# Kernel optimization log

Measured on AMD Instinct MI355X. Metric: run time of the kernel, lower is better.

The kernel has to match this reference:

```python
import jax, jax.numpy as jnp
import numpy as np


def pnp(contour, h, w):
    """Even-odd point-in-polygon rasterization.
    contour: [P, N, 2] float (x, y) pixel coords -> [P, h, w] float {0,1} masks.
    Scans over the N polygon edges (fixed structural dim), toggling parity.
    """
    P, N, _ = contour.shape
    py = jnp.arange(h, dtype=contour.dtype)[:, None]   # [h, 1]
    px = jnp.arange(w, dtype=contour.dtype)[None, :]   # [1, w]
    verts = jnp.moveaxis(contour, 1, 0)                # [N, P, 2]
    nxt = jnp.roll(verts, -1, axis=0)                  # next vertex per edge

    def step(inside, vn):
        v, n = vn
        x1 = v[:, 0][:, None, None]; y1 = v[:, 1][:, None, None]
        x2 = n[:, 0][:, None, None]; y2 = n[:, 1][:, None, None]
        crosses = (y1 > py) != (y2 > py)               # edge straddles scanline
        denom = jnp.where(y2 == y1, 1.0, y2 - y1)
        xint = (x2 - x1) * (py - y1) / denom + x1      # x of edge at scanline
        hit = crosses & (px < xint)
        return inside ^ hit, None

    inside0 = jnp.zeros((P, h, w), dtype=bool)
    inside, _ = jax.lax.scan(step, inside0, (verts, nxt))
    return inside.astype(jnp.float32)


def setup_inputs() -> dict:
    key = jax.random.key(0)
    k1, k2, k3, k4 = jax.random.split(key, 4)
    bs, c_in, h, w = 8, 64, 256, 256
    P, num_point = 40, 128
    ct_num = jax.random.randint(k1, (bs,), 1, 16)  # at least one contour per image
    cx = jax.random.uniform(k2, (P, num_point), minval=0.0, maxval=float(w - 1))
    cy = jax.random.uniform(k3, (P, num_point), minval=0.0, maxval=float(h - 1))
    contour = jnp.stack([cx, cy], axis=-1)                     # [P, N, 2]
    cnn_feature = jax.random.normal(k4, (bs, c_in, h, w), dtype=jnp.float32)
    return {"contour": contour, "cnn_feature": cnn_feature, "ct_num": ct_num}


def reference(contour, cnn_feature, ct_num):
    bs, c_in, h, w = cnn_feature.shape
    mask = pnp(contour, h, w)                                  # [P, h, w]
    max_channel = int(jnp.max(ct_num))
    # Faithful to original: slice start for batch i>=1 is ct_num[i-1] (not cumsum)
    starts = jnp.concatenate([jnp.zeros((1,), ct_num.dtype), ct_num[:-1]])
    j = jnp.arange(max_channel)
    idx = starts[:, None] + j[None, :]                         # [bs, C]
    valid = j[None, :] < ct_num[:, None]                       # [bs, C]
    gathered = mask[jnp.clip(idx, 0, mask.shape[0] - 1)]       # [bs, C, h, w]
    mask_batch = jnp.where(valid[:, :, None, None], gathered, 0.0)
    max_mask = jnp.max(mask_batch, axis=1, keepdims=True)      # [bs, 1, h, w]
    cnn_out = jax.nn.relu(max_mask * cnn_feature + cnn_feature)
    return mask_batch, cnn_out
```

## Files before the change

### kernel.cpp

```cpp
#include <hip/hip_runtime.h>

#define P_NUM 40
#define N_VERT 128
#define H 256
#define W 256
#define BS 8
#define C_IN 64
#define PIX (H * W)
#define PIX4 (PIX / 4)
#define CSPLIT 4
#define CPS (C_IN / CSPLIT)

typedef float vf2 __attribute__((ext_vector_type(2)));
typedef float vf4 __attribute__((ext_vector_type(4)));

__global__ __launch_bounds__(256) void pnp_mask_kernel(
    const float* __restrict__ contour, float* __restrict__ maskws) {
    const int p = blockIdx.x;
    const int y = blockIdx.y;
    const int tid = threadIdx.x;

    __shared__ float sx[N_VERT];
    __shared__ float sy[N_VERT];
    __shared__ float xints[N_VERT];
    __shared__ int kcnt;

    if (tid < N_VERT) {
        const vf2 v = reinterpret_cast<const vf2*>(contour)[p * N_VERT + tid];
        sx[tid] = v.x;
        sy[tid] = v.y;
    }
    if (tid == 0) kcnt = 0;
    __syncthreads();

    const float py = (float)y;
    if (tid < N_VERT) {
        const float y1 = sy[tid];
        const int e2 = (tid + 1) & (N_VERT - 1);
        const float y2 = sy[e2];
        const bool crosses = (y1 > py) != (y2 > py);
        if (crosses) {
            const float x1 = sx[tid];
            const float x2 = sx[e2];
            const float denom = (y2 == y1) ? 1.0f : (y2 - y1);
            const float xint = (x2 - x1) * (py - y1) / denom + x1;
            const int slot = atomicAdd(&kcnt, 1);
            xints[slot] = xint;
        }
    }
    __syncthreads();

    const int K = kcnt;
    const float px = (float)tid;
    int cnt = 0;
    for (int k = 0; k < K; ++k) {
        cnt += (px < xints[k]) ? 1 : 0;
    }
    maskws[(p * H + y) * W + tid] = (float)(cnt & 1);
}

__global__ __launch_bounds__(256) void mega_kernel(
    const float* __restrict__ maskws, const float* __restrict__ feat,
    const int* __restrict__ ct_num, float* __restrict__ out_mask,
    float* __restrict__ out_cnn, int C) {
    const int bid = blockIdx.x;
    const int split = bid & (CSPLIT - 1);
    const int chunk = (bid >> 2) & 63;
    const int i = bid >> 8;
    const int qv = chunk * 256 + threadIdx.x;

    const int cn = ct_num[i];
    const int start = (i == 0) ? 0 : ct_num[i - 1];

    vf4 mx = {0.f, 0.f, 0.f, 0.f};
    if (split == 0) {
        for (int j = 0; j < C; ++j) {
            vf4 m = {0.f, 0.f, 0.f, 0.f};
            if (j < cn) {
                const int p = min(max(start + j, 0), P_NUM - 1);
                m = reinterpret_cast<const vf4*>(maskws)[p * PIX4 + qv];
                mx.x = fmaxf(mx.x, m.x);
                mx.y = fmaxf(mx.y, m.y);
                mx.z = fmaxf(mx.z, m.z);
                mx.w = fmaxf(mx.w, m.w);
            }
            __builtin_nontemporal_store(
                m, reinterpret_cast<vf4*>(out_mask) + (size_t)(i * C + j) * PIX4 + qv);
        }
    } else {
        for (int j = 0; j < cn; ++j) {
            const int p = min(max(start + j, 0), P_NUM - 1);
            const vf4 m = reinterpret_cast<const vf4*>(maskws)[p * PIX4 + qv];
            mx.x = fmaxf(mx.x, m.x);
            mx.y = fmaxf(mx.y, m.y);
            mx.z = fmaxf(mx.z, m.z);
            mx.w = fmaxf(mx.w, m.w);
        }
    }

    const int cbase = split * CPS;
    for (int cc = 0; cc < CPS; ++cc) {
        const size_t idx = (size_t)(i * C_IN + cbase + cc) * PIX4 + qv;
        const vf4 f = reinterpret_cast<const vf4*>(feat)[idx];
        vf4 r;
        r.x = fmaxf(mx.x * f.x + f.x, 0.0f);
        r.y = fmaxf(mx.y * f.y + f.y, 0.0f);
        r.z = fmaxf(mx.z * f.z + f.z, 0.0f);
        r.w = fmaxf(mx.w * f.w + f.w, 0.0f);
        __builtin_nontemporal_store(r, reinterpret_cast<vf4*>(out_cnn) + idx);
    }
}

extern "C" void kernel_launch(void* const* d_in, const int* in_sizes, int n_in,
                              void* d_out, int out_size, void* d_ws, size_t ws_size,
                              hipStream_t stream) {
    const float* contour = (const float*)d_in[0];
    const float* feat = (const float*)d_in[1];
    const int* ct_num = (const int*)d_in[2];

    float* out = (float*)d_out;
    const int cnn_elems = BS * C_IN * PIX;
    const int C = (out_size - cnn_elems) / (BS * PIX);

    float* maskws = (float*)d_ws;
    float* out_mask = out;
    float* out_cnn = out + (size_t)BS * C * PIX;

    hipLaunchKernelGGL(pnp_mask_kernel, dim3(P_NUM, H), dim3(256), 0, stream,
                       contour, maskws);

    hipLaunchKernelGGL(mega_kernel, dim3(BS * 64 * CSPLIT), dim3(256), 0, stream,
                       maskws, feat, ct_num, out_mask, out_cnn, C);
}
```

Before: 65.96 us.

## Pack polygon masks into bitmasks and split mask output into separate blocks

The rasterizer now writes one bit per pixel via wavefront ballot instead of a float per pixel, which shrinks the intermediate mask workspace 32x. The fused kernel ORs the packed words to form the max mask and expands the bits back to floats. The mask_batch output is moved out of split 0 into its own set of blocks, one per (batch, channel, chunk). The channel split is raised from 4 to 8. Together these cut workspace traffic and remove the serial store loop from a subset of blocks, at the cost of bit extraction work and a larger grid.

```diff
diff --git a/kernel.cpp b/kernel.cpp
--- a/kernel.cpp
+++ b/kernel.cpp
@@ -8,14 +8,15 @@
 #define C_IN 64
 #define PIX (H * W)
 #define PIX4 (PIX / 4)
-#define CSPLIT 4
-#define CPS (C_IN / CSPLIT)
+#define CHUNKS 64
+#define ASPLIT 8
+#define CPS (C_IN / ASPLIT)
 
 typedef float vf2 __attribute__((ext_vector_type(2)));
 typedef float vf4 __attribute__((ext_vector_type(4)));
 
-__global__ __launch_bounds__(256) void pnp_mask_kernel(
-    const float* __restrict__ contour, float* __restrict__ maskws) {
+__global__ __launch_bounds__(256) void pnp_bits_kernel(
+    const float* __restrict__ contour, unsigned int* __restrict__ bitws) {
     const int p = blockIdx.x;
     const int y = blockIdx.y;
     const int tid = threadIdx.x;
@@ -56,58 +57,83 @@
     for (int k = 0; k < K; ++k) {
         cnt += (px < xints[k]) ? 1 : 0;
     }
-    maskws[(p * H + y) * W + tid] = (float)(cnt & 1);
+    const unsigned long long b = __ballot(cnt & 1);
+    if ((tid & 63) == 0) {
+        *reinterpret_cast<unsigned long long*>(
+            bitws + ((size_t)(p * H + y) << 3) + ((tid >> 6) << 1)) = b;
+    }
 }
 
-__global__ __launch_bounds__(256) void mega_kernel(
-    const float* __restrict__ maskws, const float* __restrict__ feat,
+__device__ __forceinline__ vf4 expand_bits(unsigned int word, int sh) {
+    vf4 m;
+    m.x = ((word >> (sh + 0)) & 1u) ? 1.0f : 0.0f;
+    m.y = ((word >> (sh + 1)) & 1u) ? 1.0f : 0.0f;
+    m.z = ((word >> (sh + 2)) & 1u) ? 1.0f : 0.0f;
+    m.w = ((word >> (sh + 3)) & 1u) ? 1.0f : 0.0f;
+    return m;
+}
+
+__global__ __launch_bounds__(256) void fuse_expand_kernel(
+    const unsigned int* __restrict__ bitws, const float* __restrict__ feat,
     const int* __restrict__ ct_num, float* __restrict__ out_mask,
     float* __restrict__ out_cnn, int C) {
+    const int FUSE_BLOCKS = BS * CHUNKS * ASPLIT;
     const int bid = blockIdx.x;
-    const int split = bid & (CSPLIT - 1);
-    const int chunk = (bid >> 2) & 63;
-    const int i = bid >> 8;
-    const int qv = chunk * 256 + threadIdx.x;
+    const int tid = threadIdx.x;
 
-    const int cn = ct_num[i];
-    const int start = (i == 0) ? 0 : ct_num[i - 1];
+    if (bid < FUSE_BLOCKS) {
+        const int split = bid & (ASPLIT - 1);
+        const int chunk = (bid >> 3) & (CHUNKS - 1);
+        const int i = bid >> 9;
 
-    vf4 mx = {0.f, 0.f, 0.f, 0.f};
-    if (split == 0) {
-        for (int j = 0; j < C; ++j) {
-            vf4 m = {0.f, 0.f, 0.f, 0.f};
-            if (j < cn) {
-                const int p = min(max(start + j, 0), P_NUM - 1);
-                m = reinterpret_cast<const vf4*>(maskws)[p * PIX4 + qv];
-                mx.x = fmaxf(mx.x, m.x);
-                mx.y = fmaxf(mx.y, m.y);
-                mx.z = fmaxf(mx.z, m.z);
-                mx.w = fmaxf(mx.w, m.w);
-            }
-            __builtin_nontemporal_store(
-                m, reinterpret_cast<vf4*>(out_mask) + (size_t)(i * C + j) * PIX4 + qv);
+        const int cn = ct_num[i];
+        const int start = (i == 0) ? 0 : ct_num[i - 1];
+
+        const int qv = chunk * 256 + tid;
+        const int pix = qv << 2;
+        const int y = pix >> 8;
+        const int w = (pix & 255) >> 5;
+        const int sh = pix & 31;
+
+        unsigned int orw = 0u;
+        for (int j = 0; j < cn; ++j) {
+            const int p = min(max(start + j, 0), P_NUM - 1);
+            orw |= bitws[((size_t)(p * H + y) << 3) + w];
+        }
+        const vf4 mx = expand_bits(orw, sh);
+
+        const int cbase = split * CPS;
+        for (int cc = 0; cc < CPS; ++cc) {
+            const size_t idx = ((size_t)(i * C_IN + cbase + cc) << 14) + qv;
+            const vf4 f = reinterpret_cast<const vf4*>(feat)[idx];
+            vf4 r;
+            r.x = fmaxf(mx.x * f.x + f.x, 0.0f);
+            r.y = fmaxf(mx.y * f.y + f.y, 0.0f);
+            r.z = fmaxf(mx.z * f.z + f.z, 0.0f);
+            r.w = fmaxf(mx.w * f.w + f.w, 0.0f);
+            __builtin_nontemporal_store(r, reinterpret_cast<vf4*>(out_cnn) + idx);
         }
     } else {
-        for (int j = 0; j < cn; ++j) {
+        const int b2 = bid - FUSE_BLOCKS;
+        const int chunk = b2 & (CHUNKS - 1);
+        const int ij = b2 >> 6;
+        const int i = ij / C;
+        const int j = ij - i * C;
+
+        const int qv = chunk * 256 + tid;
+        const int pix = qv << 2;
+        const int y = pix >> 8;
+        const int w = (pix & 255) >> 5;
+        const int sh = pix & 31;
+
+        vf4 m = {0.f, 0.f, 0.f, 0.f};
+        if (j < ct_num[i]) {
+            const int start = (i == 0) ? 0 : ct_num[i - 1];
             const int p = min(max(start + j, 0), P_NUM - 1);
-            const vf4 m = reinterpret_cast<const vf4*>(maskws)[p * PIX4 + qv];
-            mx.x = fmaxf(mx.x, m.x);
-            mx.y = fmaxf(mx.y, m.y);
-            mx.z = fmaxf(mx.z, m.z);
-            mx.w = fmaxf(mx.w, m.w);
+            m = expand_bits(bitws[((size_t)(p * H + y) << 3) + w], sh);
         }
-    }
-
-    const int cbase = split * CPS;
-    for (int cc = 0; cc < CPS; ++cc) {
-        const size_t idx = (size_t)(i * C_IN + cbase + cc) * PIX4 + qv;
-        const vf4 f = reinterpret_cast<const vf4*>(feat)[idx];
-        vf4 r;
-        r.x = fmaxf(mx.x * f.x + f.x, 0.0f);
-        r.y = fmaxf(mx.y * f.y + f.y, 0.0f);
-        r.z = fmaxf(mx.z * f.z + f.z, 0.0f);
-        r.w = fmaxf(mx.w * f.w + f.w, 0.0f);
-        __builtin_nontemporal_store(r, reinterpret_cast<vf4*>(out_cnn) + idx);
+        __builtin_nontemporal_store(
+            m, reinterpret_cast<vf4*>(out_mask) + ((size_t)ij << 14) + qv);
     }
 }
 
@@ -122,13 +148,16 @@
     const int cnn_elems = BS * C_IN * PIX;
     const int C = (out_size - cnn_elems) / (BS * PIX);
 
-    float* maskws = (float*)d_ws;
+    unsigned int* bitws = (unsigned int*)d_ws;
     float* out_mask = out;
     float* out_cnn = out + (size_t)BS * C * PIX;
 
-    hipLaunchKernelGGL(pnp_mask_kernel, dim3(P_NUM, H), dim3(256), 0, stream,
-                       contour, maskws);
+    hipLaunchKernelGGL(pnp_bits_kernel, dim3(P_NUM, H), dim3(256), 0, stream,
+                       contour, bitws);
 
-    hipLaunchKernelGGL(mega_kernel, dim3(BS * 64 * CSPLIT), dim3(256), 0, stream,
-                       maskws, feat, ct_num, out_mask, out_cnn, C);
+    const int fuse_blocks = BS * CHUNKS * ASPLIT;
+    const int expand_blocks = BS * C * CHUNKS;
+    hipLaunchKernelGGL(fuse_expand_kernel, dim3(fuse_blocks + expand_blocks),
+                       dim3(256), 0, stream, bitws, feat, ct_num, out_mask,
+                       out_cnn, C);
 }
```

Measured after the change: 57.03 us (median of 2 runs). 1.16x faster.
